# Performance work log

Hardware: AMD Instinct MI355X
Metric: run time of the kernel (lower is better)

## Reference

```python
import jax, jax.numpy as jnp
import numpy as np

B, C, H, W = 4, 256, 64, 64
EPS = 1e-6


def setup_inputs() -> dict:
    key = jax.random.key(0)
    ks = jax.random.split(key, 6)
    x = jax.random.normal(ks[0], (B, C, H, W), jnp.float32)
    gn_w = jnp.ones((1, C, 1, 1), jnp.float32)
    gn_b = jnp.zeros((1, C, 1, 1), jnp.float32)
    s = 1.0 / np.sqrt(C)
    w0 = jax.random.normal(ks[1], (C, C), jnp.float32) * s
    w1 = jax.random.normal(ks[2], (C, C), jnp.float32) * s
    w2 = jax.random.normal(ks[3], (C, C), jnp.float32) * s
    w3 = jax.random.normal(ks[4], (C, C), jnp.float32) * s
    b0 = jnp.zeros((C,), jnp.float32)
    b1 = jnp.zeros((C,), jnp.float32)
    b2 = jnp.zeros((C,), jnp.float32)
    b3 = jnp.zeros((C,), jnp.float32)
    return {"x": x, "gn_w": gn_w, "gn_b": gn_b,
            "w0": w0, "b0": b0, "w1": w1, "b1": b1,
            "w2": w2, "b2": b2, "w3": w3, "b3": b3}


def _nin(t, Wm, bv):
    # 1x1 conv as channel matmul: (B,C,H,W) x (C,D) -> (B,D,H,W)
    return jnp.einsum('bchw,cd->bdhw', t, Wm) + bv[None, :, None, None]


def reference(x, gn_w, gn_b, w0, b0, w1, b1, w2, b2, w3, b3):
    Bb, Cc, Hh, Ww = x.shape
    G = min(Cc // 4, 32)  # GroupLayerNorm2d groups
    # per-pixel group norm: normalize over channels within each group only
    xg = x.reshape(Bb, G, Cc // G, Hh, Ww)
    mean = xg.mean(axis=2, keepdims=True)
    var = xg.var(axis=2, keepdims=True)
    hn = ((xg - mean) / jnp.sqrt(var + EPS)).reshape(Bb, Cc, Hh, Ww)
    hn = hn * gn_w + gn_b
    q = _nin(hn, w0, b0)
    k = _nin(hn, w1, b1)
    v = _nin(hn, w2, b2)
    # full (B,H,W,H,W) scores; mask is causal along W only (key col j > query col w)
    scores = jnp.einsum('bchw,bcij->bhwij', q, k) * (float(Cc) ** -0.5)
    causal = jnp.triu(jnp.ones((Ww, Ww), bool), k=1)  # (W_query, W_key)
    scores = jnp.where(causal[None, None, :, None, :], -jnp.inf, scores)
    attn = jax.nn.softmax(scores.reshape(Bb, Hh, Ww, Hh * Ww), axis=-1)
    attn = attn.reshape(Bb, Hh, Ww, Hh, Ww)
    h = jnp.einsum('bhwij,bcij->bchw', attn, v)
    return x + _nin(h, w3, b3)  # skip_rescale=False
```

## Files before the change

### kernel.cpp

```cpp
#include <hip/hip_runtime.h>
#include <math.h>

#define LOG2E 1.4426950408889634f

typedef __attribute__((ext_vector_type(8))) __bf16 bf16x8_t;
typedef __attribute__((ext_vector_type(8))) short short8_t;
typedef __attribute__((ext_vector_type(4))) short short4_t;
typedef __attribute__((ext_vector_type(4))) float f32x4;

static __device__ __forceinline__ short f2bf(float f){
    unsigned u = __builtin_bit_cast(unsigned, f);
    unsigned r = (u + 0x7fffu + ((u >> 16) & 1u)) >> 16;
    return (short)r;
}

static __device__ __forceinline__ f32x4 mfma16(short8_t a, short8_t b, f32x4 c){
    return __builtin_amdgcn_mfma_f32_16x16x32_bf16(
        __builtin_bit_cast(bf16x8_t, a), __builtin_bit_cast(bf16x8_t, b), c, 0, 0, 0);
}

static __device__ __forceinline__ float swz16(float v){
    return __builtin_bit_cast(float,
        __builtin_amdgcn_ds_swizzle(__builtin_bit_cast(int, v), 0x401F));
}
static __device__ __forceinline__ float bperm32(int addr, float v){
    return __builtin_bit_cast(float,
        __builtin_amdgcn_ds_bpermute(addr, __builtin_bit_cast(int, v)));
}
static __device__ __forceinline__ float redmax16(f32x4 v, int a32){
    float t = fmaxf(fmaxf(v[0], v[1]), fmaxf(v[2], v[3]));
    t = fmaxf(t, swz16(t));
    t = fmaxf(t, bperm32(a32, t));
    return t;
}
static __device__ __forceinline__ float redsum16(f32x4 v, int a32){
    float t = (v[0] + v[1]) + (v[2] + v[3]);
    t += swz16(t);
    t += bperm32(a32, t);
    return t;
}

__global__ __launch_bounds__(256) void prep_w(const float* __restrict__ w0,
    const float* __restrict__ w1, const float* __restrict__ w2,
    const float* __restrict__ w3, short* __restrict__ wT)
{
    __shared__ float T[64 * 65];
    const int mat = blockIdx.x >> 4, tile = blockIdx.x & 15;
    const int c0 = (tile >> 2) * 64, d0 = (tile & 3) * 64;
    const float* src = mat == 0 ? w0 : mat == 1 ? w1 : mat == 2 ? w2 : w3;
    const int t = threadIdx.x;
    #pragma unroll
    for (int i = 0; i < 4; i++){
        int r = (t >> 4) + i * 16, c4 = (t & 15) * 4;
        f32x4 v = *(const f32x4*)(src + (size_t)(c0 + r) * 256 + d0 + c4);
        #pragma unroll
        for (int j = 0; j < 4; j++) T[r * 65 + c4 + j] = v[j];
    }
    __syncthreads();
    int drow = t >> 2, cb = (t & 3) * 16;
    short tmp[16];
    #pragma unroll
    for (int j = 0; j < 16; j++) tmp[j] = f2bf(T[(cb + j) * 65 + drow]);
    short* dst = wT + (size_t)mat * 65536 + (size_t)(d0 + drow) * 256 + c0 + cb;
    *(short8_t*)dst = *(short8_t*)tmp;
    *(short8_t*)(dst + 8) = *(short8_t*)(tmp + 8);
}

__global__ __launch_bounds__(256) void gn_kernel(const float* __restrict__ x,
    const float* __restrict__ gnw, const float* __restrict__ gnb,
    short* __restrict__ hn)
{
    int flat = blockIdx.x * 256 + threadIdx.x;
    int n = flat & 4095, g = (flat >> 12) & 31, b = flat >> 17;
    const float* xp = x + (size_t)(b * 256 + g * 8) * 4096 + n;
    float v[8], s = 0.f, s2 = 0.f;
    #pragma unroll
    for (int k = 0; k < 8; k++){ float t = xp[(size_t)k * 4096]; v[k] = t; s += t; s2 += t * t; }
    float mean = s * 0.125f;
    float var  = s2 * 0.125f - mean * mean;
    float inv  = rsqrtf(var + 1e-6f);
    int h = n >> 6, w = n & 63, m = w * 64 + h;
    short o[8];
    #pragma unroll
    for (int k = 0; k < 8; k++)
        o[k] = f2bf((v[k] - mean) * inv * gnw[g * 8 + k] + gnb[g * 8 + k]);
    *(short8_t*)(hn + (size_t)(b * 4096 + m) * 256 + g * 8) = *(short8_t*)o;
}

__global__ __launch_bounds__(256) void qkv_gemm(const short* __restrict__ hn,
    const short* __restrict__ wT, const float* __restrict__ bq,
    const float* __restrict__ bk, const float* __restrict__ bv,
    short* __restrict__ Q, short* __restrict__ Kf, short* __restrict__ Vf)
{
    __shared__ short As[64 * 72];
    __shared__ short Bs[64 * 72];
    __shared__ float CT[64 * 65];

    const int tid = threadIdx.x;
    const int m0 = blockIdx.x * 64;
    const int by = blockIdx.y;
    const int mat = by >> 2;
    const int d0 = (by & 3) * 64;
    const short* w = wT + mat * 65536;
    const float* bias = mat == 0 ? bq : mat == 1 ? bk : bv;

    const int wv = tid >> 6, lane = tid & 63;
    const int wrow = (wv >> 1) * 32, wcol = (wv & 1) * 32;
    const int lrow = lane & 15, lq = lane >> 4;

    f32x4 acc[2][2] = {};

    for (int k0 = 0; k0 < 256; k0 += 64){
        __syncthreads();
        #pragma unroll
        for (int i = 0; i < 2; i++){
            int idx = tid + i * 256, r = idx >> 3, c = (idx & 7) * 8;
            *(short8_t*)&As[r * 72 + c] = *(const short8_t*)(hn + (size_t)(m0 + r) * 256 + k0 + c);
            *(short8_t*)&Bs[r * 72 + c] = *(const short8_t*)(w  + (size_t)(d0 + r) * 256 + k0 + c);
        }
        __syncthreads();
        #pragma unroll
        for (int kk = 0; kk < 2; kk++){
            int off = kk * 32 + lq * 8;
            short8_t a0  = *(short8_t*)&As[(wrow + lrow) * 72 + off];
            short8_t a1  = *(short8_t*)&As[(wrow + 16 + lrow) * 72 + off];
            short8_t b0v = *(short8_t*)&Bs[(wcol + lrow) * 72 + off];
            short8_t b1v = *(short8_t*)&Bs[(wcol + 16 + lrow) * 72 + off];
            acc[0][0] = mfma16(a0, b0v, acc[0][0]);
            acc[0][1] = mfma16(a0, b1v, acc[0][1]);
            acc[1][0] = mfma16(a1, b0v, acc[1][0]);
            acc[1][1] = mfma16(a1, b1v, acc[1][1]);
        }
    }

    const int b = m0 >> 12, kb64 = (m0 & 4095) >> 6;

    if (mat == 0){
        #pragma unroll
        for (int i = 0; i < 2; i++)
          #pragma unroll
          for (int j = 0; j < 2; j++)
            #pragma unroll
            for (int r = 0; r < 4; r++){
                int row = wrow + i * 16 + lq * 4 + r;
                int col = wcol + j * 16 + lrow;
                Q[(size_t)(m0 + row) * 256 + d0 + col] = f2bf((acc[i][j][r] + bias[d0 + col]) * 0.0625f);
            }
    } else if (mat == 1){
        #pragma unroll
        for (int i = 0; i < 2; i++)
          #pragma unroll
          for (int j = 0; j < 2; j++)
            #pragma unroll
            for (int r = 0; r < 4; r++){
                int row = wrow + i * 16 + lq * 4 + r;
                int col = wcol + j * 16 + lrow;
                CT[row * 65 + col] = acc[i][j][r] + bias[d0 + col];
            }
        __syncthreads();
        int key = tid >> 2, c16 = (tid & 3) * 16;
        int kc = key >> 4, l15 = key & 15;
        #pragma unroll
        for (int half = 0; half < 2; half++){
            int ch0 = c16 + half * 8;
            int ks = (d0 + ch0) >> 5, lqf = (ch0 & 31) >> 3;
            short tmp[8];
            #pragma unroll
            for (int j = 0; j < 8; j++) tmp[j] = f2bf(CT[key * 65 + ch0 + j]);
            size_t base = ((((size_t)(b * 64 + kb64)) * 4 + kc) * 8 + ks) * 512 + (lqf * 16 + l15) * 8;
            *(short8_t*)(Kf + base) = *(short8_t*)tmp;
        }
    } else {
        #pragma unroll
        for (int i = 0; i < 2; i++)
          #pragma unroll
          for (int j = 0; j < 2; j++)
            #pragma unroll
            for (int r = 0; r < 4; r++){
                int row = wrow + i * 16 + lq * 4 + r;
                int col = wcol + j * 16 + lrow;
                CT[col * 65 + row] = acc[i][j][r] + bias[d0 + col];
            }
        __syncthreads();
        const int kbd = kb64 >> 1, parity = kb64 & 1;
        const int cht_l = tid >> 6, lane_s = tid & 63;
        const int l15s = lane_s & 15, lg4s = lane_s >> 4;
        const int cht = (d0 >> 4) + cht_l;
        #pragma unroll
        for (int kc = 0; kc < 4; kc++){
            short tmp[4];
            #pragma unroll
            for (int j = 0; j < 4; j++)
                tmp[j] = f2bf(CT[(cht_l * 16 + l15s) * 65 + kc * 16 + lg4s * 4 + j]);
            size_t base = (size_t)b * 1048576 + (size_t)kbd * 32768 + kc * 8192
                        + cht * 512 + lane_s * 8 + parity * 4;
            *(short4_t*)(Vf + base) = *(short4_t*)tmp;
        }
    }
}

__global__ __launch_bounds__(256, 2) void attn_kernel(const short* __restrict__ Q,
    const short* __restrict__ Kf, const short* __restrict__ Vf,
    short* __restrict__ hb)
{
    __shared__ float mls[4][16][2];
    __shared__ float LO[4][16][260];

    const int tid = threadIdx.x, lane = tid & 63, kc = tid >> 6;
    const int l15 = lane & 15, lg4 = lane >> 4;
    const int a32 = ((lane ^ 32) << 2);

    const int id = blockIdx.x;
    const int qd = id >> 8, c = id & 255;
    const int w6 = c >> 2, hh = (c >> 1) & 1, rg = c & 1;
    const int b  = qd;
    const int w  = (qd & 1) ? 63 - w6 : w6;
    const int q0 = w * 64 + hh * 32 + rg * 16;

    const short* Kb = Kf + (size_t)b * 1048576 + kc * 4096 + lane * 8;
    const short* Vb = Vf + (size_t)b * 1048576 + kc * 8192 + lane * 8;

    short8_t qf[8];
    {
        const short* qp = Q + ((size_t)b * 4096 + q0 + l15) * 256;
        #pragma unroll
        for (int ks = 0; ks < 8; ks++)
            qf[ks] = *(const short8_t*)(qp + ks * 32 + lg4 * 8);
    }

    f32x4 oacc[16] = {};
    float m_run = -1e30f, l_run = 0.f;

    short8_t kcur[8], knext[8];
    #pragma unroll
    for (int ks = 0; ks < 8; ks++)
        kcur[ks] = *(const short8_t*)(Kb + ks * 512);

    for (int kb = 0; kb <= w; kb += 2){
        const bool has_odd = (kb + 1 <= w);
        if (has_odd){
            const short* kit = Kb + (size_t)(kb + 1) * 16384;
            #pragma unroll
            for (int ks = 0; ks < 8; ks++)
                knext[ks] = *(const short8_t*)(kit + ks * 512);
        }
        f32x4 st = {};
        #pragma unroll
        for (int ks = 0; ks < 8; ks++) st = mfma16(kcur[ks], qf[ks], st);
        float mloc = redmax16(st, a32);
        float m_e = fmaxf(m_run, mloc);
        float alpha_e = exp2f((m_run - m_e) * LOG2E);
        f32x4 p_e;
        #pragma unroll
        for (int r = 0; r < 4; r++) p_e[r] = exp2f((st[r] - m_e) * LOG2E);
        l_run = l_run * alpha_e + redsum16(p_e, a32);

        f32x4 p_o = {};
        float alpha_o = 1.f;
        if (has_odd){
            if (kb + 2 <= w){
                const short* kit = Kb + (size_t)(kb + 2) * 16384;
                #pragma unroll
                for (int ks = 0; ks < 8; ks++)
                    kcur[ks] = *(const short8_t*)(kit + ks * 512);
            }
            f32x4 st2 = {};
            #pragma unroll
            for (int ks = 0; ks < 8; ks++) st2 = mfma16(knext[ks], qf[ks], st2);
            float mloc2 = redmax16(st2, a32);
            float m_o = fmaxf(m_e, mloc2);
            alpha_o = exp2f((m_e - m_o) * LOG2E);
            #pragma unroll
            for (int r = 0; r < 4; r++) p_o[r] = exp2f((st2[r] - m_o) * LOG2E);
            l_run = l_run * alpha_o + redsum16(p_o, a32);
            #pragma unroll
            for (int r = 0; r < 4; r++) p_e[r] *= alpha_o;
            m_run = m_o;
        } else {
            m_run = m_e;
        }

        short pb[8];
        #pragma unroll
        for (int r = 0; r < 4; r++){ pb[r] = f2bf(p_e[r]); pb[4 + r] = f2bf(p_o[r]); }
        short8_t pbf = *(short8_t*)pb;
        float apair = alpha_e * alpha_o;

        const short* vit = Vb + (size_t)(kb >> 1) * 32768;
        #pragma unroll
        for (int cht = 0; cht < 16; cht++){
            short8_t vfr = *(const short8_t*)(vit + cht * 512);
            f32x4 t = oacc[cht];
            #pragma unroll
            for (int r = 0; r < 4; r++) t[r] *= apair;
            oacc[cht] = mfma16(vfr, pbf, t);
        }
    }

    if (lg4 == 0){ mls[kc][l15][0] = m_run; mls[kc][l15][1] = l_run; }
    __syncthreads();
    float m0v = mls[0][l15][0], m1v = mls[1][l15][0], m2v = mls[2][l15][0], m3v = mls[3][l15][0];
    float mstar = fmaxf(fmaxf(m0v, m1v), fmaxf(m2v, m3v));
    float Lsum = mls[0][l15][1] * exp2f((m0v - mstar) * LOG2E)
               + mls[1][l15][1] * exp2f((m1v - mstar) * LOG2E)
               + mls[2][l15][1] * exp2f((m2v - mstar) * LOG2E)
               + mls[3][l15][1] * exp2f((m3v - mstar) * LOG2E);
    float sc = exp2f((m_run - mstar) * LOG2E);
    #pragma unroll
    for (int cht = 0; cht < 16; cht++){
        f32x4 t = oacc[cht];
        #pragma unroll
        for (int r = 0; r < 4; r++) t[r] *= sc;
        *(f32x4*)&LO[kc][l15][cht * 16 + lg4 * 4] = t;
    }
    __syncthreads();
    {
        const int ch0 = kc * 64 + lg4 * 16;
        float inv = 1.f / Lsum;
        f32x4 s4[4];
        #pragma unroll
        for (int c4 = 0; c4 < 4; c4++){
            f32x4 s = *(const f32x4*)&LO[0][l15][ch0 + c4 * 4];
            #pragma unroll
            for (int kcj = 1; kcj < 4; kcj++){
                f32x4 t = *(const f32x4*)&LO[kcj][l15][ch0 + c4 * 4];
                #pragma unroll
                for (int r = 0; r < 4; r++) s[r] += t[r];
            }
            #pragma unroll
            for (int r = 0; r < 4; r++) s[r] *= inv;
            s4[c4] = s;
        }
        short tmp[16];
        #pragma unroll
        for (int c4 = 0; c4 < 4; c4++)
            #pragma unroll
            for (int r = 0; r < 4; r++) tmp[c4 * 4 + r] = f2bf(s4[c4][r]);
        const int h = hh * 32 + rg * 16 + l15;
        short* dst = hb + ((size_t)b * 4096 + h * 64 + w) * 256 + ch0;
        *(short8_t*)dst = *(short8_t*)tmp;
        *(short8_t*)(dst + 8) = *(short8_t*)(tmp + 8);
    }
}

__global__ __launch_bounds__(256) void final_gemm(const short* __restrict__ hbuf,
    const short* __restrict__ wT3, const float* __restrict__ b3,
    const float* __restrict__ x, float* __restrict__ out)
{
    __shared__ short As[64 * 72];
    __shared__ short Bs[64 * 72];
    __shared__ float CT[64 * 65];

    const int tid = threadIdx.x;
    const int m0 = blockIdx.x * 64;
    const int d0 = blockIdx.y * 64;
    const int wv = tid >> 6, lane = tid & 63;
    const int wrow = (wv >> 1) * 32, wcol = (wv & 1) * 32;
    const int lrow = lane & 15, lq = lane >> 4;

    f32x4 acc[2][2] = {};
    for (int k0 = 0; k0 < 256; k0 += 64){
        __syncthreads();
        #pragma unroll
        for (int i = 0; i < 2; i++){
            int idx = tid + i * 256, r = idx >> 3, c = (idx & 7) * 8;
            *(short8_t*)&As[r * 72 + c] = *(const short8_t*)(hbuf + (size_t)(m0 + r) * 256 + k0 + c);
            *(short8_t*)&Bs[r * 72 + c] = *(const short8_t*)(wT3 + (size_t)(d0 + r) * 256 + k0 + c);
        }
        __syncthreads();
        #pragma unroll
        for (int kk = 0; kk < 2; kk++){
            int off = kk * 32 + lq * 8;
            short8_t a0  = *(short8_t*)&As[(wrow + lrow) * 72 + off];
            short8_t a1  = *(short8_t*)&As[(wrow + 16 + lrow) * 72 + off];
            short8_t b0v = *(short8_t*)&Bs[(wcol + lrow) * 72 + off];
            short8_t b1v = *(short8_t*)&Bs[(wcol + 16 + lrow) * 72 + off];
            acc[0][0] = mfma16(a0, b0v, acc[0][0]);
            acc[0][1] = mfma16(a0, b1v, acc[0][1]);
            acc[1][0] = mfma16(a1, b0v, acc[1][0]);
            acc[1][1] = mfma16(a1, b1v, acc[1][1]);
        }
    }
    #pragma unroll
    for (int i = 0; i < 2; i++)
      #pragma unroll
      for (int j = 0; j < 2; j++)
        #pragma unroll
        for (int r = 0; r < 4; r++){
            int row = wrow + i * 16 + lq * 4 + r;
            int col = wcol + j * 16 + lrow;
            CT[col * 65 + row] = acc[i][j][r] + b3[d0 + col];
        }
    __syncthreads();
    int b = m0 >> 12, n0 = m0 & 4095, hrow = n0 >> 6;
    int dr = tid >> 2, wc = (tid & 3) * 16;
    size_t base = ((size_t)(b * 256 + d0 + dr) * 64 + hrow) * 64 + wc;
    const f32x4* xp = (const f32x4*)(x + base);
    f32x4* op = (f32x4*)(out + base);
    #pragma unroll
    for (int q = 0; q < 4; q++){
        f32x4 xv = xp[q], o;
        #pragma unroll
        for (int j = 0; j < 4; j++) o[j] = xv[j] + CT[dr * 65 + wc + q * 4 + j];
        op[q] = o;
    }
}

extern "C" void kernel_launch(void* const* d_in, const int* in_sizes, int n_in,
                              void* d_out, int out_size, void* d_ws, size_t ws_size,
                              hipStream_t stream)
{
    const float* x   = (const float*)d_in[0];
    const float* gnw = (const float*)d_in[1];
    const float* gnb = (const float*)d_in[2];
    const float* w0  = (const float*)d_in[3];
    const float* b0  = (const float*)d_in[4];
    const float* w1  = (const float*)d_in[5];
    const float* b1  = (const float*)d_in[6];
    const float* w2  = (const float*)d_in[7];
    const float* b2  = (const float*)d_in[8];
    const float* w3  = (const float*)d_in[9];
    const float* b3  = (const float*)d_in[10];
    float* out = (float*)d_out;

    char* ws = (char*)d_ws;
    short* wT  = (short*)(ws);
    short* hn  = (short*)(ws + 524288);
    short* Qb  = (short*)(ws + 8912896);
    short* Kfb = (short*)(ws + 17301504);
    short* Vfb = (short*)(ws + 25690112);
    short* hb  = (short*)(ws + 34078720);

    prep_w   <<<64, 256, 0, stream>>>(w0, w1, w2, w3, wT);
    gn_kernel<<<2048, 256, 0, stream>>>(x, gnw, gnb, hn);
    qkv_gemm <<<dim3(256, 12), 256, 0, stream>>>(hn, wT, b0, b1, b2, Qb, Kfb, Vfb);
    attn_kernel<<<1024, 256, 0, stream>>>(Qb, Kfb, Vfb, hb);
    final_gemm<<<dim3(256, 4), 256, 0, stream>>>(hb, wT + 3 * 65536, b3, x, out);
}
```

Measured before the change: 230.3 us.

## Merge per-pair softmax reductions, shrink LDS to bf16, raise attention occupancy

The attention loop now computes both key-block scores before a single joint max/sum reduction per pair, replacing two sequential cross-lane reductions and two rescale factors with one. The partial-output staging buffer in LDS is stored as bf16 instead of fp32, halving shared memory. Launch bounds go from 2 to 4 blocks per SM, aiming at more latency hiding. The tighter register budget may cause spills, and bf16 staging of partial sums adds rounding error.

```diff
diff --git a/kernel.cpp b/kernel.cpp
--- a/kernel.cpp
+++ b/kernel.cpp
@@ -13,6 +13,9 @@
     unsigned r = (u + 0x7fffu + ((u >> 16) & 1u)) >> 16;
     return (short)r;
 }
+static __device__ __forceinline__ float bf2f(short s){
+    return __builtin_bit_cast(float, (unsigned)((unsigned short)s) << 16);
+}
 
 static __device__ __forceinline__ f32x4 mfma16(short8_t a, short8_t b, f32x4 c){
     return __builtin_amdgcn_mfma_f32_16x16x32_bf16(
@@ -26,18 +29,6 @@
 static __device__ __forceinline__ float bperm32(int addr, float v){
     return __builtin_bit_cast(float,
         __builtin_amdgcn_ds_bpermute(addr, __builtin_bit_cast(int, v)));
-}
-static __device__ __forceinline__ float redmax16(f32x4 v, int a32){
-    float t = fmaxf(fmaxf(v[0], v[1]), fmaxf(v[2], v[3]));
-    t = fmaxf(t, swz16(t));
-    t = fmaxf(t, bperm32(a32, t));
-    return t;
-}
-static __device__ __forceinline__ float redsum16(f32x4 v, int a32){
-    float t = (v[0] + v[1]) + (v[2] + v[3]);
-    t += swz16(t);
-    t += bperm32(a32, t);
-    return t;
 }
 
 __global__ __launch_bounds__(256) void prep_w(const float* __restrict__ w0,
@@ -199,12 +190,12 @@
     }
 }
 
-__global__ __launch_bounds__(256, 2) void attn_kernel(const short* __restrict__ Q,
+__global__ __launch_bounds__(256, 4) void attn_kernel(const short* __restrict__ Q,
     const short* __restrict__ Kf, const short* __restrict__ Vf,
     short* __restrict__ hb)
 {
     __shared__ float mls[4][16][2];
-    __shared__ float LO[4][16][260];
+    __shared__ short LOs[4][16][264];
 
     const int tid = threadIdx.x, lane = tid & 63, kc = tid >> 6;
     const int l15 = lane & 15, lg4 = lane >> 4;
@@ -247,44 +238,46 @@
         f32x4 st = {};
         #pragma unroll
         for (int ks = 0; ks < 8; ks++) st = mfma16(kcur[ks], qf[ks], st);
-        float mloc = redmax16(st, a32);
-        float m_e = fmaxf(m_run, mloc);
-        float alpha_e = exp2f((m_run - m_e) * LOG2E);
-        f32x4 p_e;
-        #pragma unroll
-        for (int r = 0; r < 4; r++) p_e[r] = exp2f((st[r] - m_e) * LOG2E);
-        l_run = l_run * alpha_e + redsum16(p_e, a32);
-
-        f32x4 p_o = {};
-        float alpha_o = 1.f;
+
+        if (kb + 2 <= w){
+            const short* kit = Kb + (size_t)(kb + 2) * 16384;
+            #pragma unroll
+            for (int ks = 0; ks < 8; ks++)
+                kcur[ks] = *(const short8_t*)(kit + ks * 512);
+        }
+
+        f32x4 st2 = { -1e30f, -1e30f, -1e30f, -1e30f };
         if (has_odd){
-            if (kb + 2 <= w){
-                const short* kit = Kb + (size_t)(kb + 2) * 16384;
-                #pragma unroll
-                for (int ks = 0; ks < 8; ks++)
-                    kcur[ks] = *(const short8_t*)(kit + ks * 512);
-            }
-            f32x4 st2 = {};
-            #pragma unroll
-            for (int ks = 0; ks < 8; ks++) st2 = mfma16(knext[ks], qf[ks], st2);
-            float mloc2 = redmax16(st2, a32);
-            float m_o = fmaxf(m_e, mloc2);
-            alpha_o = exp2f((m_e - m_o) * LOG2E);
-            #pragma unroll
-            for (int r = 0; r < 4; r++) p_o[r] = exp2f((st2[r] - m_o) * LOG2E);
-            l_run = l_run * alpha_o + redsum16(p_o, a32);
-            #pragma unroll
-            for (int r = 0; r < 4; r++) p_e[r] *= alpha_o;
-            m_run = m_o;
-        } else {
-            m_run = m_e;
-        }
+            f32x4 z = {};
+            #pragma unroll
+            for (int ks = 0; ks < 8; ks++) z = mfma16(knext[ks], qf[ks], z);
+            st2 = z;
+        }
+
+        float tmax = fmaxf(fmaxf(fmaxf(st[0], st[1]), fmaxf(st[2], st[3])),
+                           fmaxf(fmaxf(st2[0], st2[1]), fmaxf(st2[2], st2[3])));
+        tmax = fmaxf(tmax, swz16(tmax));
+        tmax = fmaxf(tmax, bperm32(a32, tmax));
+        float m_new = fmaxf(m_run, tmax);
+        float alpha = exp2f((m_run - m_new) * LOG2E);
+        m_run = m_new;
+
+        f32x4 p_e, p_o;
+        #pragma unroll
+        for (int r = 0; r < 4; r++){
+            p_e[r] = exp2f((st[r]  - m_new) * LOG2E);
+            p_o[r] = exp2f((st2[r] - m_new) * LOG2E);
+        }
+        float tsum = ((p_e[0] + p_e[1]) + (p_e[2] + p_e[3]))
+                   + ((p_o[0] + p_o[1]) + (p_o[2] + p_o[3]));
+        tsum += swz16(tsum);
+        tsum += bperm32(a32, tsum);
+        l_run = l_run * alpha + tsum;
 
         short pb[8];
         #pragma unroll
         for (int r = 0; r < 4; r++){ pb[r] = f2bf(p_e[r]); pb[4 + r] = f2bf(p_o[r]); }
         short8_t pbf = *(short8_t*)pb;
-        float apair = alpha_e * alpha_o;
 
         const short* vit = Vb + (size_t)(kb >> 1) * 32768;
         #pragma unroll
@@ -292,7 +285,7 @@
             short8_t vfr = *(const short8_t*)(vit + cht * 512);
             f32x4 t = oacc[cht];
             #pragma unroll
-            for (int r = 0; r < 4; r++) t[r] *= apair;
+            for (int r = 0; r < 4; r++) t[r] *= alpha;
             oacc[cht] = mfma16(vfr, pbf, t);
         }
     }
@@ -308,34 +301,28 @@
     float sc = exp2f((m_run - mstar) * LOG2E);
     #pragma unroll
     for (int cht = 0; cht < 16; cht++){
-        f32x4 t = oacc[cht];
-        #pragma unroll
-        for (int r = 0; r < 4; r++) t[r] *= sc;
-        *(f32x4*)&LO[kc][l15][cht * 16 + lg4 * 4] = t;
+        short t4[4];
+        #pragma unroll
+        for (int r = 0; r < 4; r++) t4[r] = f2bf(oacc[cht][r] * sc);
+        *(short4_t*)&LOs[kc][l15][cht * 16 + lg4 * 4] = *(short4_t*)t4;
     }
     __syncthreads();
     {
         const int ch0 = kc * 64 + lg4 * 16;
         float inv = 1.f / Lsum;
-        f32x4 s4[4];
-        #pragma unroll
-        for (int c4 = 0; c4 < 4; c4++){
-            f32x4 s = *(const f32x4*)&LO[0][l15][ch0 + c4 * 4];
-            #pragma unroll
-            for (int kcj = 1; kcj < 4; kcj++){
-                f32x4 t = *(const f32x4*)&LO[kcj][l15][ch0 + c4 * 4];
-                #pragma unroll
-                for (int r = 0; r < 4; r++) s[r] += t[r];
+        short tmp[16];
+        #pragma unroll
+        for (int c8 = 0; c8 < 2; c8++){
+            short8_t a0 = *(const short8_t*)&LOs[0][l15][ch0 + c8 * 8];
+            short8_t a1 = *(const short8_t*)&LOs[1][l15][ch0 + c8 * 8];
+            short8_t a2 = *(const short8_t*)&LOs[2][l15][ch0 + c8 * 8];
+            short8_t a3 = *(const short8_t*)&LOs[3][l15][ch0 + c8 * 8];
+            #pragma unroll
+            for (int j = 0; j < 8; j++){
+                float s = (bf2f(a0[j]) + bf2f(a1[j])) + (bf2f(a2[j]) + bf2f(a3[j]));
+                tmp[c8 * 8 + j] = f2bf(s * inv);
             }
-            #pragma unroll
-            for (int r = 0; r < 4; r++) s[r] *= inv;
-            s4[c4] = s;
-        }
-        short tmp[16];
-        #pragma unroll
-        for (int c4 = 0; c4 < 4; c4++)
-            #pragma unroll
-            for (int r = 0; r < 4; r++) tmp[c4 * 4 + r] = f2bf(s4[c4][r]);
+        }
         const int h = hh * 32 + rg * 16 + l15;
         short* dst = hb + ((size_t)b * 4096 + h * 64 + w) * 256 + ch0;
         *(short8_t*)dst = *(short8_t*)tmp;
```

Measured after the change: 596.3 us. +158.9%, slower.
